# Kernel optimization log

Measured on AMD Instinct MI355X. Metric: run time of the kernel, lower is better.

The kernel has to match this reference:

```python
import jax, jax.numpy as jnp
import numpy as np

K_DIFF = 2  # max_diffusion_step


def _gconv(x, supports, W, b):
    # x: (B, N, D) node features; diffusion convolution with Chebyshev-style recurrence
    mats = [x]
    for S in supports:
        x0 = x
        x1 = jnp.einsum('mn,bnd->bmd', S, x)
        mats.append(x1)
        for _ in range(2, K_DIFF + 1):
            x2 = 2.0 * jnp.einsum('mn,bnd->bmd', S, x1) - x0
            mats.append(x2)
            x0, x1 = x1, x2
    xcat = jnp.concatenate(mats, axis=-1)  # (B, N, num_matrices*D)
    return xcat @ W + b


def _dcgru_layer(seq, h0, supports, Wg, bg, Wc, bc):
    # seq: (T, B, N, D); h0: (B, N, H)
    def step(h, xt):
        ru = jax.nn.sigmoid(_gconv(jnp.concatenate([xt, h], -1), supports, Wg, bg))
        r, u = jnp.split(ru, 2, axis=-1)
        c = jnp.tanh(_gconv(jnp.concatenate([xt, r * h], -1), supports, Wc, bc))
        hn = u * h + (1.0 - u) * c
        return hn, hn
    _, out = jax.lax.scan(step, h0, seq)
    return out  # (T, B, N, H)


def setup_inputs():
    key = jax.random.key(0)
    ks = jax.random.split(key, 10)
    B, T, N, D, H, C = 32, 128, 64, 64, 64, 4
    num_mat = 2 * K_DIFF + 1
    input_seq = jax.random.normal(ks[0], (B, T, N, D), jnp.float32)
    seq_lengths = jax.random.randint(ks[1], (B,), 1, T + 1)
    A = jax.random.uniform(ks[2], (N, N), jnp.float32)
    support0 = A / A.sum(axis=1, keepdims=True)        # forward random walk
    support1 = A.T / A.T.sum(axis=1, keepdims=True)    # reverse random walk
    w = lambda k, s: jax.random.normal(k, s, jnp.float32) * 0.05
    Wg0 = w(ks[3], ((D + H) * num_mat, 2 * H)); bg0 = jnp.ones((2 * H,), jnp.float32)
    Wc0 = w(ks[4], ((D + H) * num_mat, H));     bc0 = jnp.zeros((H,), jnp.float32)
    Wg1 = w(ks[5], ((H + H) * num_mat, 2 * H)); bg1 = jnp.ones((2 * H,), jnp.float32)
    Wc1 = w(ks[6], ((H + H) * num_mat, H));     bc1 = jnp.zeros((H,), jnp.float32)
    Wp = w(ks[7], (H, C)); bp = jnp.zeros((C,), jnp.float32)
    return dict(input_seq=input_seq, seq_lengths=seq_lengths, support0=support0,
                support1=support1, Wg0=Wg0, bg0=bg0, Wc0=Wc0, bc0=bc0,
                Wg1=Wg1, bg1=bg1, Wc1=Wc1, bc1=bc1, Wp=Wp, bp=bp)


def reference(input_seq, seq_lengths, support0, support1,
              Wg0, bg0, Wc0, bc0, Wg1, bg1, Wc1, bc1, Wp, bp):
    B, T, N, D = input_seq.shape
    H = Wc0.shape[1]
    supports = (support0, support1)
    seq = jnp.transpose(input_seq, (1, 0, 2, 3))  # (T, B, N, D)
    h0 = jnp.zeros((B, N, H), input_seq.dtype)
    out0 = _dcgru_layer(seq, h0, supports, Wg0, bg0, Wc0, bc0)   # (T,B,N,H)
    out1 = _dcgru_layer(out0, h0, supports, Wg1, bg1, Wc1, bc1)  # (T,B,N,H)
    idx = jnp.clip(seq_lengths - 1, 0, T - 1)
    last = out1[idx, jnp.arange(B)]               # (B, N, H) last relevant timestep
    logits = jax.nn.relu(last) @ Wp + bp          # (B, N, C); dropout is identity (eval)
    return jnp.max(logits, axis=1)                # max-pool over nodes -> (B, C)
```

## Files before the change

kernel.cpp:

```cpp
#include <hip/hip_runtime.h>
#include <stdint.h>


typedef short short8 __attribute__((ext_vector_type(8)));
typedef float float4v __attribute__((ext_vector_type(4)));
typedef unsigned short ushort4v __attribute__((ext_vector_type(4)));
typedef unsigned int uint4v __attribute__((ext_vector_type(4)));
typedef unsigned int uint2v __attribute__((ext_vector_type(2)));

#define MF(a,b,c) __builtin_amdgcn_mfma_f32_16x16x32_bf16(a,b,c,0,0,0)

__device__ __forceinline__ unsigned short f2bf(float v){
  unsigned int x = __builtin_bit_cast(unsigned int, v);
  x += 0x7FFFu + ((x >> 16) & 1u);
  return (unsigned short)(x >> 16);
}
__device__ __forceinline__ float bf2f(unsigned short h){
  unsigned int x = ((unsigned int)h) << 16;
  return __builtin_bit_cast(float, x);
}
__device__ __forceinline__ void cvt_hilo(const float4v v, ushort4v& oh, ushort4v& ol){
#pragma unroll
  for (int r=0;r<4;r++){ unsigned short h=f2bf(v[r]); oh[r]=h; ol[r]=f2bf(v[r]-bf2f(h)); }
}

__device__ __forceinline__ unsigned int cvtpk(float a, float b){
  unsigned int r;
  asm("v_cvt_pk_bf16_f32 %0, %1, %2" : "=v"(r) : "v"(a), "v"(b));
  return r;
}
__device__ __forceinline__ float bcf(unsigned int x){
  return __builtin_bit_cast(float, x);
}
__device__ __forceinline__ void cvt_hilo_pk(const float4v v,
    unsigned int& h0, unsigned int& h1, unsigned int& l0, unsigned int& l1){
  h0 = cvtpk(v[0], v[1]);
  h1 = cvtpk(v[2], v[3]);
  l0 = cvtpk(v[0]-bcf(h0<<16), v[1]-bcf(h0&0xffff0000u));
  l1 = cvtpk(v[2]-bcf(h1<<16), v[3]-bcf(h1&0xffff0000u));
}

#define PLO 4608
#define XP  0
#define HP  9216
#define RH  18432
#define YS0 27648
#define YS1 36864
#define YS2 46080
#define YS3 55296
#define Z0F 32256
#define Z1F 36608
#define LDS_BYTES 163840

#define WSF_S2   16384
#define WSF_WG0  32768
#define WSF_WC0  196608
#define WSF_WG1  278528
#define WSF_WC1  442368
#define WSF_CAP  524288
#define WSF_FLAG 655360
#define WSF_DONE 663552
#define WSF_SLOT 663616
#define WSF_SQS  4857920

#define TB(grp,j,nt) ((((grp)*5+(j))*4+(nt))*4)

__device__ __forceinline__ void store_Y(unsigned short* lds_, int buf, int nt,
                                        int fc, int qd, const float4v* acc){
#pragma unroll
  for (int Mt=0;Mt<4;Mt++){
    unsigned int h0,h1,l0,l1;
    cvt_hilo_pk(acc[Mt],h0,h1,l0,l1);
    const int o = buf + (16*nt+fc)*72 + 16*Mt + 4*qd;
    uint2v hv; hv[0]=h0; hv[1]=h1;
    uint2v lv; lv[0]=l0; lv[1]=l1;
    *(uint2v*)(lds_+o)=hv; *(uint2v*)(lds_+o+PLO)=lv;
  }
}

__device__ __forceinline__ void xp_write_pk(unsigned short* lds_, int node, int f0,
                                            float4v a0, float4v a1){
  unsigned int h0,h1,h2,h3, l0,l1,l2,l3;
  cvt_hilo_pk(a0, h0,h1, l0,l1);
  cvt_hilo_pk(a1, h2,h3, l2,l3);
  uint4v hv; hv[0]=h0; hv[1]=h1; hv[2]=h2; hv[3]=h3;
  uint4v lv; lv[0]=l0; lv[1]=l1; lv[2]=l2; lv[3]=l3;
  *(uint4v*)(lds_ + XP + node*72 + f0) = hv;
  *(uint4v*)(lds_ + XP + PLO + node*72 + f0) = lv;
}

__device__ __forceinline__ void p1_group(unsigned short* lds_,
    const unsigned short* __restrict__ wfr, int grp, int p0, int p1,
    float bias, float4v* gacc, int w, int ln, int fc, int qd)
{
  const int nt = w & 3;
  const bool lo = (w < 4);
  float4v aY0[4], aY1[4];
#pragma unroll
  for (int Mt=0;Mt<4;Mt++){
    aY0[Mt]=(float4v){0.f,0.f,0.f,0.f};
    aY1[Mt]=(float4v){0.f,0.f,0.f,0.f};
  }
#pragma unroll
  for (int i=0;i<2;i++) gacc[i]=(float4v){bias,bias,bias,bias};
  const int tbG = TB(grp,0,nt);
  const int tbA = lo ? TB(grp,1,nt) : TB(grp,2,nt);
  const int tbB = lo ? TB(grp,3,nt) : TB(grp,4,nt);
#pragma unroll
  for (int kt=0;kt<4;kt++){
    const int pb = (kt<2)? p0 : p1;
    short8 ah[4], al[4];
#pragma unroll
    for (int Mt=0;Mt<4;Mt++){
      const int o = pb + (16*Mt+fc)*72 + 32*(kt&1) + 8*qd;
      ah[Mt]=*(const short8*)(lds_+o);
      al[Mt]=*(const short8*)(lds_+o+PLO);
    }
    {
      const unsigned short* wb = wfr + (size_t)((tbG+kt)*2)*512 + ln*8;
      short8 bh=*(const short8*)wb, bl=*(const short8*)(wb+512);
      if (lo){
        gacc[0]=MF(ah[0],bh,gacc[0]); gacc[0]=MF(ah[0],bl,gacc[0]);
        gacc[0]=MF(al[0],bh,gacc[0]);
        gacc[1]=MF(ah[1],bh,gacc[1]); gacc[1]=MF(ah[1],bl,gacc[1]);
        gacc[1]=MF(al[1],bh,gacc[1]);
      } else {
        gacc[0]=MF(ah[2],bh,gacc[0]); gacc[0]=MF(ah[2],bl,gacc[0]);
        gacc[0]=MF(al[2],bh,gacc[0]);
        gacc[1]=MF(ah[3],bh,gacc[1]); gacc[1]=MF(ah[3],bl,gacc[1]);
        gacc[1]=MF(al[3],bh,gacc[1]);
      }
    }
    {
      const unsigned short* wb = wfr + (size_t)((tbA+kt)*2)*512 + ln*8;
      short8 bh=*(const short8*)wb, bl=*(const short8*)(wb+512);
#pragma unroll
      for (int Mt=0;Mt<4;Mt++){
        aY0[Mt]=MF(ah[Mt],bh,aY0[Mt]); aY0[Mt]=MF(ah[Mt],bl,aY0[Mt]);
        aY0[Mt]=MF(al[Mt],bh,aY0[Mt]);
      }
    }
    {
      const unsigned short* wb = wfr + (size_t)((tbB+kt)*2)*512 + ln*8;
      short8 bh=*(const short8*)wb, bl=*(const short8*)(wb+512);
#pragma unroll
      for (int Mt=0;Mt<4;Mt++){
        aY1[Mt]=MF(ah[Mt],bh,aY1[Mt]); aY1[Mt]=MF(ah[Mt],bl,aY1[Mt]);
        aY1[Mt]=MF(al[Mt],bh,aY1[Mt]);
      }
    }
  }
  store_Y(lds_, lo? YS0 : YS1, nt, fc, qd, aY0);
  store_Y(lds_, lo? YS2 : YS3, nt, fc, qd, aY1);
}

__device__ __forceinline__ void p2_fused(unsigned short* lds_,
    const short8* sfA, const short8* sfB, int sup, int mt, int fc, int qd)
{
  const int ya = sup? YS2 : YS0;
  const int yb = sup? YS3 : YS1;
  float* zf = (float*)lds_ + (sup? Z1F : Z0F);
#pragma unroll
  for (int nt=0;nt<4;nt++){
    float4v acc = {0.f,0.f,0.f,0.f};
#pragma unroll
    for (int kt=0;kt<2;kt++){
      {
        const int bo = ya + (16*nt+fc)*72 + 32*kt + 8*qd;
        short8 bh=*(const short8*)(lds_+bo), bl=*(const short8*)(lds_+bo+PLO);
        acc=MF(sfA[kt*2+0],bh,acc); acc=MF(sfA[kt*2+0],bl,acc); acc=MF(sfA[kt*2+1],bh,acc);
      }
      {
        const int bo = yb + (16*nt+fc)*72 + 32*kt + 8*qd;
        short8 bh=*(const short8*)(lds_+bo), bl=*(const short8*)(lds_+bo+PLO);
        acc=MF(sfB[kt*2+0],bh,acc); acc=MF(sfB[kt*2+0],bl,acc); acc=MF(sfB[kt*2+1],bh,acc);
      }
    }
    *(float4v*)(zf + (16*nt+fc)*68 + 16*mt + 4*qd) = acc;
  }
}

__device__ __forceinline__ void read_pre(const unsigned short* lds_,
    const float4v* gacc, float4v* pre, int mo, int ntg, int fc, int qd)
{
  const float* lf = (const float*)lds_;
#pragma unroll
  for (int i=0;i<2;i++){
    const int Mt = mo+i;
    float4v za = *(const float4v*)(lf + Z0F + (16*ntg+fc)*68 + 16*Mt + 4*qd);
    float4v zb = *(const float4v*)(lf + Z1F + (16*ntg+fc)*68 + 16*Mt + 4*qd);
    pre[i] = gacc[i] + za + zb;
  }
}

__device__ __forceinline__ void scatter_plane(unsigned short* lds_, int plane,
    int mo, int ntg, int fc, int qd, const ushort4v* oh, const ushort4v* ol)
{
#pragma unroll
  for (int i=0;i<2;i++){
#pragma unroll
    for (int r=0;r<4;r++){
      const int o = plane + (16*(mo+i)+4*qd+r)*72 + 16*ntg+fc;
      lds_[o] = oh[i][r]; lds_[o+PLO] = ol[i][r];
    }
  }
}

__global__ void __launch_bounds__(512, 2)
dcrnn_main(const float* __restrict__ input_seq, const int* __restrict__ seq_lengths,
           const float* __restrict__ bg0, const float* __restrict__ bc0,
           const float* __restrict__ bg1, const float* __restrict__ bc1,
           const float* __restrict__ Wp, const float* __restrict__ bp,
           unsigned short* __restrict__ ws, float* __restrict__ out)
{
  extern __shared__ unsigned short lds_[];
  const int tid = threadIdx.x;
  const int w = tid>>6, ln = tid&63, fc = ln&15, qd = ln>>4;
  const int role = blockIdx.x >> 5;
  const int b = blockIdx.x & 31;

  const unsigned short* frags = ws;
  int* flags = (int*)(ws + WSF_FLAG) + b*128;
  int* done  = (int*)(ws + WSF_DONE) + b;
  unsigned short* capb = ws + WSF_CAP + (size_t)b*4096;
  unsigned int* slots = (unsigned int*)(ws + WSF_SLOT);

  { unsigned int* l32 = (unsigned int*)lds_;
    for (int i=4608+tid; i<9216; i+=512) l32[i]=0u; }

  const int sup = (w>>2)&1, mt = w&3;
  short8 sfA[4], sfB[4];
#pragma unroll
  for (int kt=0;kt<2;kt++)
#pragma unroll
    for (int pl=0;pl<2;pl++){
      const size_t o = (size_t)((((sup*2+pl)*4+mt)*2+kt)*512 + ln*8);
      sfA[kt*2+pl] = *(const short8*)(frags + o);
      sfB[kt*2+pl] = *(const short8*)(frags + WSF_S2 + o);
    }

  const bool lo = (w < 4);
  const int mo = lo ? 0 : 2, ntg = w & 3;
  const int gcol = 16*ntg + fc;

  const unsigned short* WGf = frags + (role? WSF_WG1 : WSF_WG0);
  const unsigned short* WCf = frags + (role? WSF_WC1 : WSF_WC0);
  const float* bg = role? bg1 : bg0;
  const float* bc = role? bc1 : bc0;
  const float brv = bg[gcol];
  const float buv = bg[64+gcol];
  const float bcv = bc[gcol];

  int tl = 0;
  if (role){ tl = seq_lengths[b]-1; tl = tl<0?0:(tl>127?127:tl); }

  float4v h_old[2], uv[2], gaccR[2], gaccU[2], gaccC[2];
#pragma unroll
  for (int i=0;i<2;i++) h_old[i]=(float4v){0.f,0.f,0.f,0.f};

  const int node8 = tid>>3, f08 = (tid&7)*8;
  float4v v_nxt0 = {0.f,0.f,0.f,0.f}, v_nxt1 = {0.f,0.f,0.f,0.f};
  __syncthreads();

  if (role==0){
    const float* s0 = input_seq + (((size_t)b*128 + 0)*64 + node8)*64 + f08;
    float4v a0 = *(const float4v*)(s0);
    float4v a1 = *(const float4v*)(s0+4);
    xp_write_pk(lds_, node8, f08, a0, a1);
    const float* s1 = input_seq + (((size_t)b*128 + 1)*64 + node8)*64 + f08;
    v_nxt0 = *(const float4v*)(s1); v_nxt1 = *(const float4v*)(s1+4);
    __syncthreads();
  } else {
    if (tid==0){
      while (__hip_atomic_load(&flags[0], __ATOMIC_ACQUIRE, __HIP_MEMORY_SCOPE_AGENT) != 1)
        __builtin_amdgcn_s_sleep(1);
      __threadfence();
    }
    __syncthreads();
    {
      const unsigned int* sl = slots + ((size_t)(b*16 + 0))*4096 + (w*64+ln)*8;
#pragma unroll
      for (int i=0;i<2;i++){
        uint4v v = *(const uint4v*)(sl + i*4);
#pragma unroll
        for (int r=0;r<4;r++){
          const int o = XP + (16*(mo+i)+4*qd+r)*72 + gcol;
          lds_[o] = (unsigned short)(v[r] & 0xffffu);
          lds_[o+PLO] = (unsigned short)(v[r] >> 16);
        }
      }
    }
    __syncthreads();
    if (tid==0)
      __hip_atomic_store(done, 1, __ATOMIC_RELEASE, __HIP_MEMORY_SCOPE_AGENT);
  }

#pragma unroll 1
  for (int t=0; t<128; ++t){
    p1_group(lds_, WGf, 0, XP, HP, brv, gaccR, w, ln, fc, qd);
    __syncthreads();
    p2_fused(lds_, sfA, sfB, sup, mt, fc, qd);
    __syncthreads();

    p1_group(lds_, WGf, 1, XP, HP, buv, gaccU, w, ln, fc, qd);
    {
      float4v pre[2]; read_pre(lds_, gaccR, pre, mo, ntg, fc, qd);
      ushort4v oh[2], ol[2];
#pragma unroll
      for (int i=0;i<2;i++){
        float4v rh;
#pragma unroll
        for (int r=0;r<4;r++){
          float rv = 1.f/(1.f+__expf(-pre[i][r]));
          rh[r] = rv*h_old[i][r];
        }
        unsigned int h0,h1,l0,l1;
        cvt_hilo_pk(rh, h0,h1, l0,l1);
        oh[i][0]=(unsigned short)h0; oh[i][1]=(unsigned short)(h0>>16);
        oh[i][2]=(unsigned short)h1; oh[i][3]=(unsigned short)(h1>>16);
        ol[i][0]=(unsigned short)l0; ol[i][1]=(unsigned short)(l0>>16);
        ol[i][2]=(unsigned short)l1; ol[i][3]=(unsigned short)(l1>>16);
      }
      scatter_plane(lds_, RH, mo, ntg, fc, qd, oh, ol);
    }
    __syncthreads();
    p2_fused(lds_, sfA, sfB, sup, mt, fc, qd);
    __syncthreads();

    p1_group(lds_, WCf, 0, XP, RH, bcv, gaccC, w, ln, fc, qd);
    {
      float4v pre[2]; read_pre(lds_, gaccU, pre, mo, ntg, fc, qd);
#pragma unroll
      for (int i=0;i<2;i++)
#pragma unroll
        for (int r=0;r<4;r++) uv[i][r] = 1.f/(1.f+__expf(-pre[i][r]));
    }
    __syncthreads();

    if (role==0){
      if (t<127) xp_write_pk(lds_, node8, f08, v_nxt0, v_nxt1);
      p2_fused(lds_, sfA, sfB, sup, mt, fc, qd);
      if (tid==0 && t>=16){
        while ((int)__hip_atomic_load(done, __ATOMIC_ACQUIRE, __HIP_MEMORY_SCOPE_AGENT) < t-15)
          __builtin_amdgcn_s_sleep(1);
      }
    } else {
      p2_fused(lds_, sfA, sfB, sup, mt, fc, qd);
      if (tid==0 && t<127){
        while (__hip_atomic_load(&flags[t+1], __ATOMIC_ACQUIRE, __HIP_MEMORY_SCOPE_AGENT) != t+2)
          __builtin_amdgcn_s_sleep(1);
        __threadfence();
      }
    }
    __syncthreads();

    {
      uint4v sv0, sv1;
      sv0[0]=0;sv0[1]=0;sv0[2]=0;sv0[3]=0; sv1=sv0;
      if (role && t<127){
        const unsigned int* sl = slots + ((size_t)(b*16 + ((t+1)&15)))*4096 + (w*64+ln)*8;
        sv0 = *(const uint4v*)(sl);
        sv1 = *(const uint4v*)(sl + 4);
      }
      if (role==0 && t<126){
        const float* s2 = input_seq + (((size_t)b*128 + (t+2))*64 + node8)*64 + f08;
        v_nxt0 = *(const float4v*)(s2); v_nxt1 = *(const float4v*)(s2+4);
      }
      float4v pre[2]; read_pre(lds_, gaccC, pre, mo, ntg, fc, qd);
      ushort4v oh[2], ol[2];
#pragma unroll
      for (int i=0;i<2;i++){
        float4v hn;
#pragma unroll
        for (int r=0;r<4;r++){
          float x = fminf(pre[i][r], 15.f);
          float e = __expf(2.f*x);
          float cv = (e-1.f)/(e+1.f);
          float u1 = uv[i][r];
          hn[r] = u1*h_old[i][r] + (1.f-u1)*cv;
        }
        h_old[i] = hn;
        cvt_hilo(hn, oh[i], ol[i]);
      }
      scatter_plane(lds_, HP, mo, ntg, fc, qd, oh, ol);
      if (role==0){
        unsigned int* sl = slots + ((size_t)(b*16 + (t&15)))*4096 + (w*64+ln)*8;
#pragma unroll
        for (int i=0;i<2;i++){
          uint4v pk;
#pragma unroll
          for (int r=0;r<4;r++)
            pk[r] = (unsigned int)oh[i][r] | ((unsigned int)ol[i][r] << 16);
          *(uint4v*)(sl + i*4) = pk;
        }
      } else {
        if (t==tl){
#pragma unroll
          for (int i=0;i<2;i++)
#pragma unroll
            for (int r=0;r<4;r++)
              capb[(16*(mo+i)+4*qd+r)*64 + gcol] = oh[i][r];
        }
        if (t<127){
#pragma unroll
          for (int i=0;i<2;i++){
            uint4v v = i ? sv1 : sv0;
#pragma unroll
            for (int r=0;r<4;r++){
              const int o = XP + (16*(mo+i)+4*qd+r)*72 + gcol;
              lds_[o] = (unsigned short)(v[r] & 0xffffu);
              lds_[o+PLO] = (unsigned short)(v[r] >> 16);
            }
          }
        }
      }
    }
    __syncthreads();
    if (tid==0){
      if (role==0){
        __threadfence();
        __hip_atomic_store(&flags[t], t+1, __ATOMIC_RELEASE, __HIP_MEMORY_SCOPE_AGENT);
      } else if (t<127){
        __hip_atomic_store(done, t+2, __ATOMIC_RELEASE, __HIP_MEMORY_SCOPE_AGENT);
      }
    }
  }

  if (role==0) return;

  __threadfence();
  __syncthreads();
  float* sc = (float*)lds_;
  if (tid < 64){
    const unsigned short* hpx = capb + tid*64;
    float4v acc = {bp[0], bp[1], bp[2], bp[3]};
#pragma unroll 1
    for (int ch = 0; ch < 64; ++ch){
      float h = fmaxf(bf2f(hpx[ch]), 0.f);
      const float4v wr = *(const float4v*)(Wp + ch*4);
      acc += h * wr;
    }
    sc[tid*4+0]=acc[0]; sc[tid*4+1]=acc[1]; sc[tid*4+2]=acc[2]; sc[tid*4+3]=acc[3];
  }
  __syncthreads();
  if (tid < 4){
    float m = sc[tid];
#pragma unroll 1
    for (int n=1;n<64;n++) m = fmaxf(m, sc[n*4 + tid]);
    out[b*4 + tid] = m;
  }
}

__global__ void __launch_bounds__(256)
dcrnn_sq(const float* __restrict__ S0, const float* __restrict__ S1,
         float* __restrict__ sqs)
{
  const float* S = blockIdx.x ? S1 : S0;
  float* D = sqs + blockIdx.x*4096;
  const int i = threadIdx.x >> 2, j0 = (threadIdx.x & 3)*16;
  float acc[16];
#pragma unroll
  for (int j=0;j<16;j++) acc[j]=0.f;
#pragma unroll 4
  for (int k=0;k<64;k++){
    float s = S[i*64+k];
    const float* row = S + k*64 + j0;
#pragma unroll
    for (int j=0;j<16;j++) acc[j] += s*row[j];
  }
#pragma unroll
  for (int j=0;j<16;j++) D[i*64+j0+j]=acc[j];
}

__global__ void __launch_bounds__(256)
dcrnn_prep(const float* __restrict__ S0, const float* __restrict__ S1,
           const float* __restrict__ Wg0, const float* __restrict__ Wc0,
           const float* __restrict__ Wg1, const float* __restrict__ Wc1,
           const float* __restrict__ sqs, unsigned short* __restrict__ frags)
{
  const int uid = blockIdx.x*256 + threadIdx.x;
  if (uid >= 65536) return;
  short8 o;
  unsigned short* dst;
  if (uid < 4096){
    int r = uid & 2047;
    const bool issq = uid >= 2048;
    const int lane = r & 63; r >>= 6;
    const int kt = r & 1; r >>= 1;
    const int Mt = r & 3; r >>= 2;
    const int pl = r & 1; r >>= 1;
    const float* S = issq ? (sqs + r*4096) : (r ? S1 : S0);
    const int m  = 16*Mt + (lane & 15);
    const int k0 = 32*kt + 8*(lane >> 4);
#pragma unroll
    for (int j=0;j<8;j++){
      float v = S[m*64 + k0 + j];
      unsigned short hi = f2bf(v);
      o[j] = (short)(pl ? f2bf(v - bf2f(hi)) : hi);
    }
    dst = frags + (issq ? WSF_S2 : 0) + (size_t)(uid & 2047)*8;
  } else {
    int u2 = uid - 4096;
    const float* W; int wld; size_t base;
    if      (u2 < 20480){ W = Wg0; wld = 128; base = WSF_WG0; }
    else if (u2 < 30720){ W = Wc0; wld = 64;  base = WSF_WC0; u2 -= 20480; }
    else if (u2 < 51200){ W = Wg1; wld = 128; base = WSF_WG1; u2 -= 30720; }
    else                { W = Wc1; wld = 64;  base = WSF_WC1; u2 -= 51200; }
    const int lane = u2 & 63;
    const int pl   = (u2 >> 6) & 1;
    const int rest = u2 >> 7;
    const int kt = rest & 3;
    const int nt = (rest >> 2) & 3;
    const int j  = (rest >> 4) % 5;
    const int grp= (rest >> 4) / 5;
    const int col = grp*64 + 16*nt + (lane & 15);
    const int k0  = 32*kt + 8*(lane >> 4);
#pragma unroll
    for (int jj=0;jj<8;jj++){
      const int k = k0 + jj;
      float v;
      if (j == 0)
        v = W[(size_t)k*wld + col] - W[(size_t)(256+k)*wld + col] - W[(size_t)(512+k)*wld + col];
      else {
        v = W[(size_t)(j*128 + k)*wld + col];
        if (j == 2 || j == 4) v *= 2.f;
      }
      unsigned short hi = f2bf(v);
      o[jj] = (short)(pl ? f2bf(v - bf2f(hi)) : hi);
    }
    dst = frags + base + (size_t)u2*8;
  }
  *(short8*)dst = o;
}

extern "C" void kernel_launch(void* const* d_in, const int* in_sizes, int n_in,
                              void* d_out, int out_size, void* d_ws, size_t ws_size,
                              hipStream_t stream) {
  const float* input_seq   = (const float*)d_in[0];
  const int*   seq_lengths = (const int*)  d_in[1];
  const float* S0  = (const float*)d_in[2];
  const float* S1  = (const float*)d_in[3];
  const float* Wg0 = (const float*)d_in[4];
  const float* bg0 = (const float*)d_in[5];
  const float* Wc0 = (const float*)d_in[6];
  const float* bc0 = (const float*)d_in[7];
  const float* Wg1 = (const float*)d_in[8];
  const float* bg1 = (const float*)d_in[9];
  const float* Wc1 = (const float*)d_in[10];
  const float* bc1 = (const float*)d_in[11];
  const float* Wp  = (const float*)d_in[12];
  const float* bp  = (const float*)d_in[13];

  unsigned short* ws = (unsigned short*)d_ws;
  float* sqs = (float*)(ws + WSF_SQS);

  dcrnn_sq<<<dim3(2), dim3(256), 0, stream>>>(S0, S1, sqs);
  dcrnn_prep<<<dim3(256), dim3(256), 0, stream>>>(S0, S1, Wg0, Wc0, Wg1, Wc1, sqs, ws);

  (void)hipFuncSetAttribute((const void*)dcrnn_main,
                            hipFuncAttributeMaxDynamicSharedMemorySize, LDS_BYTES);
  dcrnn_main<<<dim3(64), dim3(512), LDS_BYTES, stream>>>(
      input_seq, seq_lengths, bg0, bc0, bg1, bc1, Wp, bp, ws, (float*)d_out);
}
```

Baseline: 2.441 ms.

## Add four helper waves to split phase-1 diffusion GEMM work across 12 waves

Grows the block from 8 to 12 waves. The four new waves take over the YS2/YS3 support projections in p1_group, so the original 8 waves each do only the gate and one Y projection. The intent is to cut the per-wave MFMA chain length in the serial recurrent step. The extra waves skip p2, the activations and the I/O, but they still join every barrier. This raises register pressure under the new launch bounds, and whether the tail section also needs guards is not visible.

```diff
diff --git a/kernel.cpp b/kernel.cpp
--- a/kernel.cpp
+++ b/kernel.cpp
@@ -94,18 +94,19 @@
     float bias, float4v* gacc, int w, int ln, int fc, int qd)
 {
   const int nt = w & 3;
-  const bool lo = (w < 4);
   float4v aY0[4], aY1[4];
 #pragma unroll
   for (int Mt=0;Mt<4;Mt++){
     aY0[Mt]=(float4v){0.f,0.f,0.f,0.f};
     aY1[Mt]=(float4v){0.f,0.f,0.f,0.f};
   }
-#pragma unroll
-  for (int i=0;i<2;i++) gacc[i]=(float4v){bias,bias,bias,bias};
+  if (w < 8){
+#pragma unroll
+    for (int i=0;i<2;i++) gacc[i]=(float4v){bias,bias,bias,bias};
+  }
   const int tbG = TB(grp,0,nt);
-  const int tbA = lo ? TB(grp,1,nt) : TB(grp,2,nt);
-  const int tbB = lo ? TB(grp,3,nt) : TB(grp,4,nt);
+  const int tbA = (w<4)? TB(grp,1,nt) : (w<8)? TB(grp,2,nt) : TB(grp,3,nt);
+  const int tbB = TB(grp,4,nt);
 #pragma unroll
   for (int kt=0;kt<4;kt++){
     const int pb = (kt<2)? p0 : p1;
@@ -116,42 +117,60 @@
       ah[Mt]=*(const short8*)(lds_+o);
       al[Mt]=*(const short8*)(lds_+o+PLO);
     }
-    {
-      const unsigned short* wb = wfr + (size_t)((tbG+kt)*2)*512 + ln*8;
-      short8 bh=*(const short8*)wb, bl=*(const short8*)(wb+512);
-      if (lo){
-        gacc[0]=MF(ah[0],bh,gacc[0]); gacc[0]=MF(ah[0],bl,gacc[0]);
-        gacc[0]=MF(al[0],bh,gacc[0]);
-        gacc[1]=MF(ah[1],bh,gacc[1]); gacc[1]=MF(ah[1],bl,gacc[1]);
-        gacc[1]=MF(al[1],bh,gacc[1]);
-      } else {
-        gacc[0]=MF(ah[2],bh,gacc[0]); gacc[0]=MF(ah[2],bl,gacc[0]);
-        gacc[0]=MF(al[2],bh,gacc[0]);
-        gacc[1]=MF(ah[3],bh,gacc[1]); gacc[1]=MF(ah[3],bl,gacc[1]);
-        gacc[1]=MF(al[3],bh,gacc[1]);
-      }
-    }
-    {
-      const unsigned short* wb = wfr + (size_t)((tbA+kt)*2)*512 + ln*8;
-      short8 bh=*(const short8*)wb, bl=*(const short8*)(wb+512);
-#pragma unroll
-      for (int Mt=0;Mt<4;Mt++){
-        aY0[Mt]=MF(ah[Mt],bh,aY0[Mt]); aY0[Mt]=MF(ah[Mt],bl,aY0[Mt]);
-        aY0[Mt]=MF(al[Mt],bh,aY0[Mt]);
-      }
-    }
-    {
-      const unsigned short* wb = wfr + (size_t)((tbB+kt)*2)*512 + ln*8;
-      short8 bh=*(const short8*)wb, bl=*(const short8*)(wb+512);
-#pragma unroll
-      for (int Mt=0;Mt<4;Mt++){
-        aY1[Mt]=MF(ah[Mt],bh,aY1[Mt]); aY1[Mt]=MF(ah[Mt],bl,aY1[Mt]);
-        aY1[Mt]=MF(al[Mt],bh,aY1[Mt]);
-      }
-    }
-  }
-  store_Y(lds_, lo? YS0 : YS1, nt, fc, qd, aY0);
-  store_Y(lds_, lo? YS2 : YS3, nt, fc, qd, aY1);
+    if (w < 8){
+      {
+        const unsigned short* wb = wfr + (size_t)((tbG+kt)*2)*512 + ln*8;
+        short8 bh=*(const short8*)wb, bl=*(const short8*)(wb+512);
+        if (w < 4){
+          gacc[0]=MF(ah[0],bh,gacc[0]); gacc[0]=MF(ah[0],bl,gacc[0]);
+          gacc[0]=MF(al[0],bh,gacc[0]);
+          gacc[1]=MF(ah[1],bh,gacc[1]); gacc[1]=MF(ah[1],bl,gacc[1]);
+          gacc[1]=MF(al[1],bh,gacc[1]);
+        } else {
+          gacc[0]=MF(ah[2],bh,gacc[0]); gacc[0]=MF(ah[2],bl,gacc[0]);
+          gacc[0]=MF(al[2],bh,gacc[0]);
+          gacc[1]=MF(ah[3],bh,gacc[1]); gacc[1]=MF(ah[3],bl,gacc[1]);
+          gacc[1]=MF(al[3],bh,gacc[1]);
+        }
+      }
+      {
+        const unsigned short* wb = wfr + (size_t)((tbA+kt)*2)*512 + ln*8;
+        short8 bh=*(const short8*)wb, bl=*(const short8*)(wb+512);
+#pragma unroll
+        for (int Mt=0;Mt<4;Mt++){
+          aY0[Mt]=MF(ah[Mt],bh,aY0[Mt]); aY0[Mt]=MF(ah[Mt],bl,aY0[Mt]);
+          aY0[Mt]=MF(al[Mt],bh,aY0[Mt]);
+        }
+      }
+    } else {
+      {
+        const unsigned short* wb = wfr + (size_t)((tbA+kt)*2)*512 + ln*8;
+        short8 bh=*(const short8*)wb, bl=*(const short8*)(wb+512);
+#pragma unroll
+        for (int Mt=0;Mt<4;Mt++){
+          aY0[Mt]=MF(ah[Mt],bh,aY0[Mt]); aY0[Mt]=MF(ah[Mt],bl,aY0[Mt]);
+          aY0[Mt]=MF(al[Mt],bh,aY0[Mt]);
+        }
+      }
+      {
+        const unsigned short* wb = wfr + (size_t)((tbB+kt)*2)*512 + ln*8;
+        short8 bh=*(const short8*)wb, bl=*(const short8*)(wb+512);
+#pragma unroll
+        for (int Mt=0;Mt<4;Mt++){
+          aY1[Mt]=MF(ah[Mt],bh,aY1[Mt]); aY1[Mt]=MF(ah[Mt],bl,aY1[Mt]);
+          aY1[Mt]=MF(al[Mt],bh,aY1[Mt]);
+        }
+      }
+    }
+  }
+  if (w < 4){
+    store_Y(lds_, YS0, nt, fc, qd, aY0);
+  } else if (w < 8){
+    store_Y(lds_, YS1, nt, fc, qd, aY0);
+  } else {
+    store_Y(lds_, YS2, nt, fc, qd, aY0);
+    store_Y(lds_, YS3, nt, fc, qd, aY1);
+  }
 }
 
 __device__ __forceinline__ void p2_fused(unsigned short* lds_,
@@ -206,7 +225,7 @@
   }
 }
 
-__global__ void __launch_bounds__(512, 2)
+__global__ void __launch_bounds__(768, 3)
 dcrnn_main(const float* __restrict__ input_seq, const int* __restrict__ seq_lengths,
            const float* __restrict__ bg0, const float* __restrict__ bc0,
            const float* __restrict__ bg1, const float* __restrict__ bc1,
@@ -218,6 +237,7 @@
   const int w = tid>>6, ln = tid&63, fc = ln&15, qd = ln>>4;
   const int role = blockIdx.x >> 5;
   const int b = blockIdx.x & 31;
+  const bool core = (w < 8);
 
   const unsigned short* frags = ws;
   int* flags = (int*)(ws + WSF_FLAG) + b*128;
@@ -226,18 +246,20 @@
   unsigned int* slots = (unsigned int*)(ws + WSF_SLOT);
 
   { unsigned int* l32 = (unsigned int*)lds_;
-    for (int i=4608+tid; i<9216; i+=512) l32[i]=0u; }
+    for (int i=4608+tid; i<9216; i+=768) l32[i]=0u; }
 
   const int sup = (w>>2)&1, mt = w&3;
   short8 sfA[4], sfB[4];
-#pragma unroll
-  for (int kt=0;kt<2;kt++)
-#pragma unroll
-    for (int pl=0;pl<2;pl++){
-      const size_t o = (size_t)((((sup*2+pl)*4+mt)*2+kt)*512 + ln*8);
-      sfA[kt*2+pl] = *(const short8*)(frags + o);
-      sfB[kt*2+pl] = *(const short8*)(frags + WSF_S2 + o);
-    }
+  if (core){
+#pragma unroll
+    for (int kt=0;kt<2;kt++)
+#pragma unroll
+      for (int pl=0;pl<2;pl++){
+        const size_t o = (size_t)((((sup*2+pl)*4+mt)*2+kt)*512 + ln*8);
+        sfA[kt*2+pl] = *(const short8*)(frags + o);
+        sfB[kt*2+pl] = *(const short8*)(frags + WSF_S2 + o);
+      }
+  }
 
   const bool lo = (w < 4);
   const int mo = lo ? 0 : 2, ntg = w & 3;
@@ -263,12 +285,14 @@
   __syncthreads();
 
   if (role==0){
-    const float* s0 = input_seq + (((size_t)b*128 + 0)*64 + node8)*64 + f08;
-    float4v a0 = *(const float4v*)(s0);
-    float4v a1 = *(const float4v*)(s0+4);
-    xp_write_pk(lds_, node8, f08, a0, a1);
-    const float* s1 = input_seq + (((size_t)b*128 + 1)*64 + node8)*64 + f08;
-    v_nxt0 = *(const float4v*)(s1); v_nxt1 = *(const float4v*)(s1+4);
+    if (core){
+      const float* s0 = input_seq + (((size_t)b*128 + 0)*64 + node8)*64 + f08;
+      float4v a0 = *(const float4v*)(s0);
+      float4v a1 = *(const float4v*)(s0+4);
+      xp_write_pk(lds_, node8, f08, a0, a1);
+      const float* s1 = input_seq + (((size_t)b*128 + 1)*64 + node8)*64 + f08;
+      v_nxt0 = *(const float4v*)(s1); v_nxt1 = *(const float4v*)(s1+4);
+    }
     __syncthreads();
   } else {
     if (tid==0){
@@ -277,7 +301,7 @@
       __threadfence();
     }
     __syncthreads();
-    {
+    if (core){
       const unsigned int* sl = slots + ((size_t)(b*16 + 0))*4096 + (w*64+ln)*8;
 #pragma unroll
       for (int i=0;i<2;i++){
@@ -299,11 +323,11 @@
   for (int t=0; t<128; ++t){
     p1_group(lds_, WGf, 0, XP, HP, brv, gaccR, w, ln, fc, qd);
     __syncthreads();
-    p2_fused(lds_, sfA, sfB, sup, mt, fc, qd);
+    if (core) p2_fused(lds_, sfA, sfB, sup, mt, fc, qd);
     __syncthreads();
 
     p1_group(lds_, WGf, 1, XP, HP, buv, gaccU, w, ln, fc, qd);
-    {
+    if (core){
       float4v pre[2]; read_pre(lds_, gaccR, pre, mo, ntg, fc, qd);
       ushort4v oh[2], ol[2];
 #pragma unroll
@@ -324,11 +348,11 @@
       scatter_plane(lds_, RH, mo, ntg, fc, qd, oh, ol);
     }
     __syncthreads();
-    p2_fused(lds_, sfA, sfB, sup, mt, fc, qd);
+    if (core) p2_fused(lds_, sfA, sfB, sup, mt, fc, qd);
     __syncthreads();
 
     p1_group(lds_, WCf, 0, XP, RH, bcv, gaccC, w, ln, fc, qd);
-    {
+    if (core){
       float4v pre[2]; read_pre(lds_, gaccU, pre, mo, ntg, fc, qd);
 #pragma unroll
       for (int i=0;i<2;i++)
@@ -338,14 +362,14 @@
     __syncthreads();
 
     if (role==0){
-      if (t<127) xp_write_pk(lds_, node8, f08, v_nxt0, v_nxt1);
-      p2_fused(lds_, sfA, sfB, sup, mt, fc, qd);
+      if (core && t<127) xp_write_pk(lds_, node8, f08, v_nxt0, v_nxt1);
+      if (core) p2_fused(lds_, sfA, sfB, sup, mt, fc, qd);
       if (tid==0 && t>=16){
         while ((int)__hip_atomic_load(done, __ATOMIC_ACQUIRE, __HIP_MEMORY_SCOPE_AGENT) < t-15)
           __builtin_amdgcn_s_sleep(1);
       }
     } else {
-      p2_fused(lds_, sfA, sfB, sup, mt, fc, qd);
+      if (core) p2_fused(lds_, sfA, sfB, sup, mt, fc, qd);
       if (tid==0 && t<127){
         while (__hip_atomic_load(&flags[t+1], __ATOMIC_ACQUIRE, __HIP_MEMORY_SCOPE_AGENT) != t+2)
           __builtin_amdgcn_s_sleep(1);
@@ -354,7 +378,7 @@
     }
     __syncthreads();
 
-    {
+    if (core){
       uint4v sv0, sv1;
       sv0[0]=0;sv0[1]=0;sv0[2]=0;sv0[3]=0; sv1=sv0;
       if (role && t<127){
@@ -559,6 +583,6 @@
 
   (void)hipFuncSetAttribute((const void*)dcrnn_main,
                             hipFuncAttributeMaxDynamicSharedMemorySize, LDS_BYTES);
-  dcrnn_main<<<dim3(64), dim3(512), LDS_BYTES, stream>>>(
+  dcrnn_main<<<dim3(64), dim3(768), LDS_BYTES, stream>>>(
       input_seq, seq_lengths, bg0, bc0, bg1, bc1, Wp, bp, ws, (float*)d_out);
 }
```

Measured after the change: 3.289 ms. 34.7% more time.
